# Kernel optimization log

Hardware: AMD Instinct MI355X
Metric: run time of the kernel (lower is better)

Reference implementation:

```python
import jax, jax.numpy as jnp
import numpy as np

D_MODEL, D_STATE, D_CONV, D_INNER = 1024, 16, 4, 2048
B, S = 1, 2048
EPS = 1e-5


def setup_inputs() -> dict:
    key = jax.random.key(0)
    ks = jax.random.split(key, 8)
    sc = 0.02
    return {
        "x": jax.random.normal(ks[0], (B, S, D_MODEL), jnp.float32),
        "ln_g": jnp.ones((D_MODEL,), jnp.float32),
        "ln_b": jnp.zeros((D_MODEL,), jnp.float32),
        "in_w": jax.random.normal(ks[1], (2 * D_INNER, D_MODEL), jnp.float32) * sc,
        "conv_w": jax.random.normal(ks[2], (D_INNER, 1, D_CONV), jnp.float32) * sc,  # depthwise OIH
        "conv_b": jax.random.normal(ks[3], (D_INNER,), jnp.float32) * sc,
        "xproj_w": jax.random.normal(ks[4], (2 * D_STATE + 1, D_INNER), jnp.float32) * sc,
        "dt_w": jax.random.normal(ks[5], (D_INNER, 1), jnp.float32) * sc,
        "dt_b": jax.random.normal(ks[6], (D_INNER,), jnp.float32) * sc,
        "A_log": jnp.log(jnp.arange(1, D_STATE + 1, dtype=jnp.float32)),
        "D": jnp.ones((D_INNER,), jnp.float32),
        "out_w": jax.random.normal(ks[7], (D_MODEL, D_INNER), jnp.float32) * sc,
    }


def reference(x, ln_g, ln_b, in_w, conv_w, conv_b, xproj_w, dt_w, dt_b, A_log, D, out_w):
    b, s, _ = x.shape
    d_inner = D.shape[0]
    d_state = A_log.shape[0]
    d_conv = conv_w.shape[-1]
    residual = x

    # LayerNorm
    mu = jnp.mean(x, axis=-1, keepdims=True)
    var = jnp.mean(jnp.square(x - mu), axis=-1, keepdims=True)
    xn = (x - mu) * jax.lax.rsqrt(var + EPS) * ln_g + ln_b

    # in_proj, split into x and gate z
    xz = jnp.einsum('bsd,ed->bse', xn, in_w)  # [B,S,2*d_inner]
    xi, z = jnp.split(xz, 2, axis=-1)

    # causal depthwise conv1d (torch pads d_conv-1 both sides then crops to seq_len)
    xc = jnp.transpose(xi, (0, 2, 1))  # [B,C,S]
    xc = jnp.pad(xc, ((0, 0), (0, 0), (d_conv - 1, 0)))
    xc = jax.lax.conv_general_dilated(
        xc, conv_w, window_strides=(1,), padding='VALID',
        dimension_numbers=('NCH', 'OIH', 'NCH'), feature_group_count=d_inner)
    xc = xc + conv_b[None, :, None]
    xs = jax.nn.silu(jnp.transpose(xc, (0, 2, 1)))  # [B,S,d_inner]

    # SSM projections
    xp = jnp.einsum('bsd,ed->bse', xs, xproj_w)  # [B,S,2*d_state+1]
    delta = jax.nn.softplus(xp[..., :1] * dt_w[:, 0] + dt_b)  # [B,S,d_inner]
    Bm = xp[..., 1:1 + d_state]  # [B,S,N]
    Cm = xp[..., 1 + d_state:]   # [B,S,N]
    A = -jnp.exp(A_log)          # [N]

    dA = jnp.exp(delta[..., None] * A)                      # [B,S,d_inner,N]
    dBx = delta[..., None] * Bm[:, :, None, :] * xs[..., None]  # [B,S,d_inner,N]

    def step(h, inp):
        dA_t, dBx_t, C_t = inp
        h = dA_t * h + dBx_t                     # [B,d_inner,N]
        y_t = jnp.einsum('bdn,bn->bd', h, C_t)   # [B,d_inner]
        return h, y_t

    h0 = jnp.zeros((b, d_inner, d_state), x.dtype)
    _, ys = jax.lax.scan(step, h0, (jnp.moveaxis(dA, 1, 0),
                                    jnp.moveaxis(dBx, 1, 0),
                                    jnp.moveaxis(Cm, 1, 0)))
    y = jnp.moveaxis(ys, 0, 1) + xs * D  # [B,S,d_inner]

    y = y * jax.nn.silu(z)
    out = jnp.einsum('bse,de->bsd', y, out_w)
    return out + residual
```

## Files before the change

kernel.cpp:

```cpp
#include <hip/hip_runtime.h>
#include <cstdint>
#include <cstddef>

#define D_MODEL 1024
#define D_STATE 16
#define D_CONV  4
#define D_INNER 2048
#define SEQ     2048
#define NCHUNK  128
#define CLEN    16
#define NGRP    8
#define GCH     16
#define LN_EPS  1e-5f

typedef unsigned short ushort_t;
typedef __attribute__((ext_vector_type(8))) short short8;
typedef __attribute__((ext_vector_type(4))) float f32x4;

__device__ __forceinline__ ushort_t f2bf(float x) {
  union { float f; uint32_t u; } v; v.f = x;
  uint32_t r = (v.u + 0x7fffu + ((v.u >> 16) & 1u)) >> 16;
  return (ushort_t)r;
}
__device__ __forceinline__ float bf2f(ushort_t u) {
  union { uint32_t x; float f; } v; v.x = ((uint32_t)u) << 16; return v.f;
}

__device__ __forceinline__ void async16(void* lds, const void* g) {
  __builtin_amdgcn_global_load_lds(
      (const __attribute__((address_space(1))) unsigned int*)g,
      (__attribute__((address_space(3))) unsigned int*)lds, 16, 0, 0);
}

__device__ __forceinline__ float softplus_f(float x) {
  if (x > 20.f) return x;
  if (x < -20.f) return __expf(x);
  return __logf(1.f + __expf(x));
}

__device__ __forceinline__ void dapow(float g1, float* da) {
  float g2 = g1 * g1, g4 = g2 * g2, g8 = g4 * g4;
  #pragma unroll
  for (int n = 0; n < 16; n++) {
    int e = n + 1;
    float v = (e & 1) ? g1 : 1.f;
    if (e & 2) v *= g2;
    if (e & 4) v *= g4;
    if (e & 8) v *= g8;
    da[n] = v;
  }
}

__global__ __launch_bounds__(256) void prep_kernel(const float* __restrict__ x,
                                                   const float* __restrict__ g,
                                                   const float* __restrict__ b,
                                                   const float* __restrict__ inw,
                                                   const float* __restrict__ outw,
                                                   const float* __restrict__ xpw,
                                                   ushort_t* __restrict__ xn_bf,
                                                   ushort_t* __restrict__ inw_bf,
                                                   ushort_t* __restrict__ outw_bf,
                                                   ushort_t* __restrict__ xpw_bf) {
  int blk = blockIdx.x;
  if (blk < SEQ) {
    int row = blk;
    const float4* xr = (const float4*)(x + (size_t)row * D_MODEL);
    float4 v = xr[threadIdx.x];
    float s  = v.x + v.y + v.z + v.w;
    float ss = v.x * v.x + v.y * v.y + v.z * v.z + v.w * v.w;
    #pragma unroll
    for (int o = 32; o; o >>= 1) { s += __shfl_down(s, o); ss += __shfl_down(ss, o); }
    __shared__ float sbuf[8], ssbuf[8];
    int wid = threadIdx.x >> 6, lane = threadIdx.x & 63;
    if (lane == 0) { sbuf[wid] = s; ssbuf[wid] = ss; }
    __syncthreads();
    if (threadIdx.x == 0) {
      float t = 0.f, t2 = 0.f;
      for (int i = 0; i < 4; i++) { t += sbuf[i]; t2 += ssbuf[i]; }
      float mu = t / D_MODEL;
      sbuf[4] = mu;
      ssbuf[4] = rsqrtf(t2 / D_MODEL - mu * mu + LN_EPS);
    }
    __syncthreads();
    float mu = sbuf[4], inv = ssbuf[4];
    float4 gv = ((const float4*)g)[threadIdx.x];
    float4 bv = ((const float4*)b)[threadIdx.x];
    ushort_t o4[4];
    o4[0] = f2bf((v.x - mu) * inv * gv.x + bv.x);
    o4[1] = f2bf((v.y - mu) * inv * gv.y + bv.y);
    o4[2] = f2bf((v.z - mu) * inv * gv.z + bv.z);
    o4[3] = f2bf((v.w - mu) * inv * gv.w + bv.w);
    *(ushort4*)&xn_bf[(size_t)row * D_MODEL + threadIdx.x * 4] =
        make_ushort4(o4[0], o4[1], o4[2], o4[3]);
  } else {
    int idx = ((blk - SEQ) * 256 + threadIdx.x) * 4;
    const int n1 = 2 * D_INNER * D_MODEL;
    const int n2 = D_MODEL * D_INNER;
    const int n3 = 64 * D_INNER;
    const float* src; ushort_t* dst; int j;
    if (idx < n1) { src = inw; dst = inw_bf; j = idx; }
    else if (idx < n1 + n2) { src = outw; dst = outw_bf; j = idx - n1; }
    else if (idx < n1 + n2 + n3) {
      j = idx - n1 - n2;
      if (j < 33 * D_INNER) { src = xpw; dst = xpw_bf; }
      else {
        *(ushort4*)&xpw_bf[j] = make_ushort4(0, 0, 0, 0);
        return;
      }
    } else return;
    float4 v = *(const float4*)&src[j];
    *(ushort4*)&dst[j] = make_ushort4(f2bf(v.x), f2bf(v.y), f2bf(v.z), f2bf(v.w));
  }
}

template <int BM, int BN, int KDIM, int EPI, int NBUF, int KSPLIT>
__global__ __launch_bounds__(256, 2) void gemm_pipe(const ushort_t* __restrict__ A,
                                                    const ushort_t* __restrict__ B,
                                                    void* __restrict__ Cout,
                                                    const float* __restrict__ R,
                                                    int N) {
  constexpr int KT = KDIM / 32 / KSPLIT;
  constexpr int K2 = KDIM * 2;
  constexpr int IA = BM / 64, IB = BN / 64;
  constexpr int S  = IA + IB;
  constexpr int W  = (NBUF - 2) * S;
  constexpr int WTM = BM / 2, WTN = BN / 2;
  constexpr int MREP = WTM / 16, NREP = WTN / 16;
  __shared__ __align__(16) ushort_t As[NBUF][BM * 32];
  __shared__ __align__(16) ushort_t Bs[NBUF][BN * 32];

  const int nwg = gridDim.x * gridDim.y;
  int bid = blockIdx.y * gridDim.x + blockIdx.x;
  int swz = (bid & 7) * (nwg >> 3) + (bid >> 3);
  int bn = swz % gridDim.x, bm = swz / gridDim.x;
  int ks = 0;
  if constexpr (KSPLIT > 1) { ks = bn; bn = 0; }
  const int tid = threadIdx.x, wid = tid >> 6, lane = tid & 63;
  const int wm = wid >> 1, wn = wid & 1;
  const int row0A = bm * BM, row0B = bn * BN;
  const size_t kbase = (size_t)ks * KT * 64;

  const char* gA[IA];
  const char* gB[IB];
  #pragma unroll
  for (int i = 0; i < IA; i++) {
    int o = i * 4096 + tid * 16;
    int r = o >> 6, src = (o & 63) ^ ((r & 3) << 4);
    gA[i] = (const char*)A + (size_t)(row0A + r) * K2 + src + kbase;
  }
  #pragma unroll
  for (int i = 0; i < IB; i++) {
    int o = i * 4096 + tid * 16;
    int r = o >> 6, src = (o & 63) ^ ((r & 3) << 4);
    gB[i] = (const char*)B + (size_t)(row0B + r) * K2 + src + kbase;
  }
  const int ldsW = wid * 1024;

  auto STAGE = [&](int bb, int kt) {
    int kb = kt * 64;
    #pragma unroll
    for (int i = 0; i < IA; i++)
      async16((char*)&As[bb][0] + i * 4096 + ldsW, gA[i] + kb);
    #pragma unroll
    for (int i = 0; i < IB; i++)
      async16((char*)&Bs[bb][0] + i * 4096 + ldsW, gB[i] + kb);
  };

  #pragma unroll
  for (int p = 0; p < NBUF - 1; p++) STAGE(p, p);

  int offA[MREP], offB[NREP];
  #pragma unroll
  for (int m = 0; m < MREP; m++) {
    int row = wm * WTM + m * 16 + (lane & 15);
    offA[m] = row * 64 + ((((lane >> 4)) ^ (row & 3)) << 4);
  }
  #pragma unroll
  for (int n = 0; n < NREP; n++) {
    int row = wn * WTN + n * 16 + (lane & 15);
    offB[n] = row * 64 + ((((lane >> 4)) ^ (row & 3)) << 4);
  }

  f32x4 acc[MREP][NREP] = {};
  int cur = 0;
  for (int kt = 0; kt < KT; kt++) {
    if (kt < KT - 1) {
      if constexpr (W == 6)       asm volatile("s_waitcnt vmcnt(6)" ::: "memory");
      else if constexpr (W == 8)  asm volatile("s_waitcnt vmcnt(8)" ::: "memory");
      else if constexpr (W == 12) asm volatile("s_waitcnt vmcnt(12)" ::: "memory");
      else                        asm volatile("s_waitcnt vmcnt(0)" ::: "memory");
    } else {
      asm volatile("s_waitcnt vmcnt(0)" ::: "memory");
    }
    __builtin_amdgcn_s_barrier();
    __builtin_amdgcn_sched_barrier(0);
    const char* Ab = (const char*)&As[cur][0];
    const char* Bb = (const char*)&Bs[cur][0];
    short8 af[MREP], bf[NREP];
    #pragma unroll
    for (int m = 0; m < MREP; m++) af[m] = *(const short8*)(Ab + offA[m]);
    #pragma unroll
    for (int n = 0; n < NREP; n++) bf[n] = *(const short8*)(Bb + offB[n]);
    if (kt + NBUF - 1 < KT) {
      int b2 = cur + NBUF - 1; if (b2 >= NBUF) b2 -= NBUF;
      STAGE(b2, kt + NBUF - 1);
    }
    __builtin_amdgcn_s_setprio(1);
    #pragma unroll
    for (int m = 0; m < MREP; m++)
      #pragma unroll
      for (int n = 0; n < NREP; n++)
        acc[m][n] = __builtin_amdgcn_mfma_f32_16x16x32_bf16(af[m], bf[n], acc[m][n], 0, 0, 0);
    __builtin_amdgcn_s_setprio(0);
    cur++; if (cur == NBUF) cur = 0;
  }

  #pragma unroll
  for (int m = 0; m < MREP; m++)
    #pragma unroll
    for (int n = 0; n < NREP; n++) {
      int r0 = row0A + wm * WTM + m * 16 + ((lane >> 4) << 2);
      int c  = row0B + wn * WTN + n * 16 + (lane & 15);
      #pragma unroll
      for (int q = 0; q < 4; q++) {
        if constexpr (EPI == 0) {
          ((ushort_t*)Cout)[(size_t)(r0 + q) * N + c] = f2bf(acc[m][n][q]);
        } else if constexpr (EPI == 1) {
          size_t idx = (size_t)(r0 + q) * N + c;
          ((float*)Cout)[idx] = acc[m][n][q] + R[idx];
        } else {
          if (c < 33)
            ((float*)Cout)[((size_t)ks * SEQ + r0 + q) * 33 + c] = acc[m][n][q];
        }
      }
    }
}

__global__ __launch_bounds__(256) void conv_silu_kernel(const ushort_t* __restrict__ xz_bf,
                                                        const float* __restrict__ cw,
                                                        const float* __restrict__ cb,
                                                        ushort_t* __restrict__ xs_bf) {
  const int t0 = blockIdx.x * 4;
  const int d0 = threadIdx.x * 8;
  short8 win[7];
  #pragma unroll
  for (int j = 0; j < 7; j++) {
    int tt = t0 - 3 + j;
    if (tt >= 0) win[j] = *(const short8*)&xz_bf[(size_t)tt * (2 * D_INNER) + d0];
    else         win[j] = (short8)0;
  }
  float4 w[8];
  float  cbv[8];
  #pragma unroll
  for (int j = 0; j < 8; j++) { w[j] = ((const float4*)cw)[d0 + j]; cbv[j] = cb[d0 + j]; }
  #pragma unroll
  for (int q = 0; q < 4; q++) {
    short8 o8;
    #pragma unroll
    for (int j = 0; j < 8; j++) {
      float acc = cbv[j]
                + bf2f((ushort_t)win[q][j])     * w[j].x
                + bf2f((ushort_t)win[q + 1][j]) * w[j].y
                + bf2f((ushort_t)win[q + 2][j]) * w[j].z
                + bf2f((ushort_t)win[q + 3][j]) * w[j].w;
      float sg = 1.f / (1.f + __expf(-acc));
      o8[j] = (short)f2bf(acc * sg);
    }
    *(short8*)&xs_bf[(size_t)(t0 + q) * D_INNER + d0] = o8;
  }
}

__global__ __launch_bounds__(256) void scan_pass1(const ushort_t* __restrict__ xs_bf,
                                                  const float* __restrict__ xpp,
                                                  const float* __restrict__ dt_w,
                                                  const float* __restrict__ dt_b,
                                                  const float* __restrict__ A_log,
                                                  ushort_t* __restrict__ Hp,
                                                  float* __restrict__ Sd) {
  int c = blockIdx.x;
  int d0 = blockIdx.y * 512 + threadIdx.x;
  __shared__ float Bsh[CLEN][16], drs[CLEN], Ash[16];
  {
    int t = threadIdx.x >> 4, n = threadIdx.x & 15;
    const size_t P = (size_t)SEQ * 33;
    size_t rb = (size_t)(c * CLEN + t) * 33;
    float sB = 0.f;
    #pragma unroll
    for (int k = 0; k < 8; k++) sB += xpp[k * P + rb + 1 + n];
    Bsh[t][n] = sB;
    if (threadIdx.x < CLEN) {
      size_t rr = (size_t)(c * CLEN + threadIdx.x) * 33;
      float sD = 0.f;
      #pragma unroll
      for (int k = 0; k < 8; k++) sD += xpp[k * P + rr];
      drs[threadIdx.x] = sD;
    } else if (threadIdx.x < CLEN + 16) {
      int n2 = threadIdx.x - CLEN;
      Ash[n2] = -__expf(A_log[n2]);
    }
  }
  __syncthreads();
  bool fastA = true;
  #pragma unroll
  for (int n = 0; n < 16; n++) fastA = fastA && (fabsf(Ash[n] + (float)(n + 1)) < 1e-4f * (n + 1));
  float dw[2] = {dt_w[d0], dt_w[d0 + 256]};
  float db[2] = {dt_b[d0], dt_b[d0 + 256]};
  float h[2][16] = {};
  float S[2] = {0.f, 0.f};
  size_t tb = (size_t)(c * CLEN) * D_INNER + d0;
  float xv[2] = {bf2f(xs_bf[tb]), bf2f(xs_bf[tb + 256])};
  for (int t = 0; t < CLEN; t++) {
    float nx[2] = {0.f, 0.f};
    if (t + 1 < CLEN) {
      nx[0] = bf2f(xs_bf[tb + D_INNER]);
      nx[1] = bf2f(xs_bf[tb + D_INNER + 256]);
    }
    float bb[16];
    *(float4*)&bb[0]  = *(const float4*)&Bsh[t][0];
    *(float4*)&bb[4]  = *(const float4*)&Bsh[t][4];
    *(float4*)&bb[8]  = *(const float4*)&Bsh[t][8];
    *(float4*)&bb[12] = *(const float4*)&Bsh[t][12];
    float drt = drs[t];
    #pragma unroll
    for (int u = 0; u < 2; u++) {
      float delta = softplus_f(drt * dw[u] + db[u]);
      S[u] += delta;
      float w = delta * xv[u];
      if (fastA) {
        float da[16];
        dapow(__expf(-delta), da);
        #pragma unroll
        for (int n = 0; n < 16; n++) h[u][n] = da[n] * h[u][n] + w * bb[n];
      } else {
        #pragma unroll
        for (int n = 0; n < 16; n++) h[u][n] = __expf(delta * Ash[n]) * h[u][n] + w * bb[n];
      }
    }
    xv[0] = nx[0]; xv[1] = nx[1];
    tb += D_INNER;
  }
  #pragma unroll
  for (int u = 0; u < 2; u++) {
    int d = d0 + u * 256;
    size_t base = ((size_t)c * D_INNER + d) * 16;
    short8 p0, p1;
    #pragma unroll
    for (int n = 0; n < 8; n++) { p0[n] = (short)f2bf(h[u][n]); p1[n] = (short)f2bf(h[u][8 + n]); }
    *(short8*)&Hp[base] = p0;
    *(short8*)&Hp[base + 8] = p1;
    Sd[(size_t)c * D_INNER + d] = S[u];
  }
}

__global__ __launch_bounds__(256) void combineA(const ushort_t* __restrict__ Hp,
                                                const float* __restrict__ Sd,
                                                const float* __restrict__ A_log,
                                                ushort_t* __restrict__ Hl,
                                                float* __restrict__ Slocp,
                                                ushort_t* __restrict__ Hgtot,
                                                float* __restrict__ Sgtot) {
  int g = blockIdx.x;
  int idx = blockIdx.y * 256 + threadIdx.x;
  int d = idx >> 4, n = idx & 15;
  float An = -__expf(A_log[n]);
  float h = 0.f, S = 0.f;
  const size_t stride = (size_t)D_INNER * 16;
  #pragma unroll 4
  for (int j = 0; j < GCH; j++) {
    int c = g * GCH + j;
    Hl[(size_t)c * stride + idx] = f2bf(h);
    if (n == 0) Slocp[(size_t)c * D_INNER + d] = S;
    float Sc = Sd[(size_t)c * D_INNER + d];
    float hp = bf2f(Hp[(size_t)c * stride + idx]);
    h = __expf(An * Sc) * h + hp;
    S += Sc;
  }
  Hgtot[(size_t)g * stride + idx] = f2bf(h);
  if (n == 0) Sgtot[(size_t)g * D_INNER + d] = S;
}

__global__ __launch_bounds__(256) void combineB(const ushort_t* __restrict__ Hgtot,
                                                const float* __restrict__ Sgtot,
                                                const float* __restrict__ A_log,
                                                ushort_t* __restrict__ Ginit) {
  int idx = blockIdx.x * 256 + threadIdx.x;
  int d = idx >> 4, n = idx & 15;
  float An = -__expf(A_log[n]);
  float G = 0.f;
  const size_t stride = (size_t)D_INNER * 16;
  #pragma unroll
  for (int g = 0; g < NGRP; g++) {
    Ginit[(size_t)g * stride + idx] = f2bf(G);
    G = __expf(An * Sgtot[(size_t)g * D_INNER + d]) * G + bf2f(Hgtot[(size_t)g * stride + idx]);
  }
}

__global__ __launch_bounds__(256) void scan_pass2(const ushort_t* __restrict__ xs_bf,
                                                  const float* __restrict__ xpp,
                                                  const ushort_t* __restrict__ xz_bf,
                                                  const float* __restrict__ dt_w,
                                                  const float* __restrict__ dt_b,
                                                  const float* __restrict__ A_log,
                                                  const float* __restrict__ Dp,
                                                  const ushort_t* __restrict__ Hl,
                                                  const float* __restrict__ Slocp,
                                                  const ushort_t* __restrict__ Ginit,
                                                  ushort_t* __restrict__ y_bf) {
  int c = blockIdx.x;
  int d0 = blockIdx.y * 512 + threadIdx.x;
  __shared__ float Bsh[CLEN][16], Csh[CLEN][16], drs[CLEN], Ash[16];
  {
    int t = threadIdx.x >> 4, n = threadIdx.x & 15;
    const size_t P = (size_t)SEQ * 33;
    size_t rb = (size_t)(c * CLEN + t) * 33;
    float sB = 0.f, sC = 0.f;
    #pragma unroll
    for (int k = 0; k < 8; k++) {
      sB += xpp[k * P + rb + 1 + n];
      sC += xpp[k * P + rb + 17 + n];
    }
    Bsh[t][n] = sB;
    Csh[t][n] = sC;
    if (threadIdx.x < CLEN) {
      size_t rr = (size_t)(c * CLEN + threadIdx.x) * 33;
      float sD = 0.f;
      #pragma unroll
      for (int k = 0; k < 8; k++) sD += xpp[k * P + rr];
      drs[threadIdx.x] = sD;
    } else if (threadIdx.x < CLEN + 16) {
      int n2 = threadIdx.x - CLEN;
      Ash[n2] = -__expf(A_log[n2]);
    }
  }
  __syncthreads();
  bool fastA = true;
  #pragma unroll
  for (int n = 0; n < 16; n++) fastA = fastA && (fabsf(Ash[n] + (float)(n + 1)) < 1e-4f * (n + 1));
  float dw[2] = {dt_w[d0], dt_w[d0 + 256]};
  float db[2] = {dt_b[d0], dt_b[d0 + 256]};
  float Dd[2] = {Dp[d0], Dp[d0 + 256]};
  int g8 = c >> 4;
  float h[2][16];
  #pragma unroll
  for (int u = 0; u < 2; u++) {
    int d = d0 + u * 256;
    size_t hb = ((size_t)c * D_INNER + d) * 16;
    size_t gb = ((size_t)g8 * D_INNER + d) * 16;
    float Slp = Slocp[(size_t)c * D_INNER + d];
    short8 hl0 = *(const short8*)&Hl[hb];
    short8 hl1 = *(const short8*)&Hl[hb + 8];
    short8 gi0 = *(const short8*)&Ginit[gb];
    short8 gi1 = *(const short8*)&Ginit[gb + 8];
    float hl[16], gi[16];
    #pragma unroll
    for (int n = 0; n < 8; n++) {
      hl[n] = bf2f((ushort_t)hl0[n]); hl[8 + n] = bf2f((ushort_t)hl1[n]);
      gi[n] = bf2f((ushort_t)gi0[n]); gi[8 + n] = bf2f((ushort_t)gi1[n]);
    }
    if (fastA) {
      float pw[16];
      dapow(__expf(-Slp), pw);
      #pragma unroll
      for (int n = 0; n < 16; n++) h[u][n] = hl[n] + pw[n] * gi[n];
    } else {
      #pragma unroll
      for (int n = 0; n < 16; n++) h[u][n] = hl[n] + __expf(Ash[n] * Slp) * gi[n];
    }
  }
  size_t tb = (size_t)(c * CLEN) * D_INNER + d0;
  size_t zb = (size_t)(c * CLEN) * (2 * D_INNER) + D_INNER + d0;
  float xv[2] = {bf2f(xs_bf[tb]), bf2f(xs_bf[tb + 256])};
  float zv[2] = {bf2f(xz_bf[zb]), bf2f(xz_bf[zb + 256])};
  for (int t = 0; t < CLEN; t++) {
    float nx[2] = {0.f, 0.f}, nz[2] = {0.f, 0.f};
    if (t + 1 < CLEN) {
      nx[0] = bf2f(xs_bf[tb + D_INNER]);
      nx[1] = bf2f(xs_bf[tb + D_INNER + 256]);
      nz[0] = bf2f(xz_bf[zb + 2 * D_INNER]);
      nz[1] = bf2f(xz_bf[zb + 2 * D_INNER + 256]);
    }
    float bb[16], cc[16];
    *(float4*)&bb[0]  = *(const float4*)&Bsh[t][0];
    *(float4*)&bb[4]  = *(const float4*)&Bsh[t][4];
    *(float4*)&bb[8]  = *(const float4*)&Bsh[t][8];
    *(float4*)&bb[12] = *(const float4*)&Bsh[t][12];
    *(float4*)&cc[0]  = *(const float4*)&Csh[t][0];
    *(float4*)&cc[4]  = *(const float4*)&Csh[t][4];
    *(float4*)&cc[8]  = *(const float4*)&Csh[t][8];
    *(float4*)&cc[12] = *(const float4*)&Csh[t][12];
    float drt = drs[t];
    size_t ti = (size_t)(c * CLEN + t);
    #pragma unroll
    for (int u = 0; u < 2; u++) {
      float delta = softplus_f(drt * dw[u] + db[u]);
      float w = delta * xv[u];
      float y = 0.f;
      if (fastA) {
        float da[16];
        dapow(__expf(-delta), da);
        #pragma unroll
        for (int n = 0; n < 16; n++) {
          h[u][n] = da[n] * h[u][n] + w * bb[n];
          y += h[u][n] * cc[n];
        }
      } else {
        #pragma unroll
        for (int n = 0; n < 16; n++) {
          h[u][n] = __expf(delta * Ash[n]) * h[u][n] + w * bb[n];
          y += h[u][n] * cc[n];
        }
      }
      float z = zv[u];
      float sz = z / (1.f + __expf(-z));
      float out = (y + xv[u] * Dd[u]) * sz;
      y_bf[ti * D_INNER + d0 + u * 256] = f2bf(out);
    }
    xv[0] = nx[0]; xv[1] = nx[1];
    zv[0] = nz[0]; zv[1] = nz[1];
    tb += D_INNER; zb += 2 * D_INNER;
  }
}

extern "C" void kernel_launch(void* const* d_in, const int* in_sizes, int n_in,
                              void* d_out, int out_size, void* d_ws, size_t ws_size,
                              hipStream_t stream) {
  const float* x      = (const float*)d_in[0];
  const float* ln_g   = (const float*)d_in[1];
  const float* ln_b   = (const float*)d_in[2];
  const float* in_w   = (const float*)d_in[3];
  const float* conv_w = (const float*)d_in[4];
  const float* conv_b = (const float*)d_in[5];
  const float* xproj_w= (const float*)d_in[6];
  const float* dt_w   = (const float*)d_in[7];
  const float* dt_b   = (const float*)d_in[8];
  const float* A_log  = (const float*)d_in[9];
  const float* Dp     = (const float*)d_in[10];
  const float* out_w  = (const float*)d_in[11];
  float* out = (float*)d_out;

  char* ws = (char*)d_ws;
  size_t off = 0;
  auto alloc = [&](size_t bytes) { char* p = ws + off; off += (bytes + 255) & ~(size_t)255; return p; };
  ushort_t* xz_bf   = (ushort_t*)alloc((size_t)SEQ * 2 * D_INNER * 2);
  ushort_t* xn_bf   = (ushort_t*)alloc((size_t)SEQ * D_MODEL * 2);
  ushort_t* inw_bf  = (ushort_t*)alloc((size_t)2 * D_INNER * D_MODEL * 2);
  ushort_t* outw_bf = (ushort_t*)alloc((size_t)D_MODEL * D_INNER * 2);
  ushort_t* xpw_bf  = (ushort_t*)alloc((size_t)64 * D_INNER * 2);
  ushort_t* xs_bf   = (ushort_t*)alloc((size_t)SEQ * D_INNER * 2);
  float*    xp_part = (float*)   alloc((size_t)8 * SEQ * 33 * 4);
  ushort_t* Hp      = (ushort_t*)alloc((size_t)NCHUNK * D_INNER * 16 * 2);
  ushort_t* Hl      = (ushort_t*)alloc((size_t)NCHUNK * D_INNER * 16 * 2);
  float*    Sd      = (float*)   alloc((size_t)NCHUNK * D_INNER * 4);
  float*    Slocp   = (float*)   alloc((size_t)NCHUNK * D_INNER * 4);
  ushort_t* Hgtot   = (ushort_t*)alloc((size_t)NGRP * D_INNER * 16 * 2);
  float*    Sgtot   = (float*)   alloc((size_t)NGRP * D_INNER * 4);
  ushort_t* Ginit   = (ushort_t*)alloc((size_t)NGRP * D_INNER * 16 * 2);
  ushort_t* y_bf    = (ushort_t*)alloc((size_t)SEQ * D_INNER * 2);
  (void)ws_size;

  const int ncvt4 = (2 * D_INNER * D_MODEL + D_MODEL * D_INNER + 64 * D_INNER) / 4;
  prep_kernel<<<SEQ + (ncvt4 + 255) / 256, 256, 0, stream>>>(
      x, ln_g, ln_b, in_w, out_w, xproj_w, xn_bf, inw_bf, outw_bf, xpw_bf);
  gemm_pipe<128, 128, D_MODEL, 0, 4, 1><<<dim3(2 * D_INNER / 128, SEQ / 128), 256, 0, stream>>>(
      xn_bf, inw_bf, xz_bf, nullptr, 2 * D_INNER);
  conv_silu_kernel<<<SEQ / 4, 256, 0, stream>>>(xz_bf, conv_w, conv_b, xs_bf);
  gemm_pipe<64, 64, D_INNER, 3, 6, 8><<<dim3(8, SEQ / 64), 256, 0, stream>>>(
      xs_bf, xpw_bf, xp_part, nullptr, 64);
  scan_pass1<<<dim3(NCHUNK, D_INNER / 512), 256, 0, stream>>>(xs_bf, xp_part, dt_w, dt_b, A_log, Hp, Sd);
  combineA<<<dim3(NGRP, D_INNER * 16 / 256), 256, 0, stream>>>(Hp, Sd, A_log, Hl, Slocp, Hgtot, Sgtot);
  combineB<<<D_INNER * 16 / 256, 256, 0, stream>>>(Hgtot, Sgtot, A_log, Ginit);
  scan_pass2<<<dim3(NCHUNK, D_INNER / 512), 256, 0, stream>>>(xs_bf, xp_part, xz_bf, dt_w, dt_b, A_log,
                                                              Dp, Hl, Slocp, Ginit, y_bf);
  gemm_pipe<64, 64, D_INNER, 1, 6, 1><<<dim3(D_MODEL / 64, SEQ / 64), 256, 0, stream>>>(
      y_bf, outw_bf, out, x, D_MODEL);
}
```

Before: 118.7 us.

## Fuse conv+SiLU into x_proj GEMM and fold combineB into scan_pass2

Measured after the change: 124.7 us. 1.05x slower.

```diff
diff --git a/kernel.cpp b/kernel.cpp
--- a/kernel.cpp
+++ b/kernel.cpp
@@ -225,49 +225,115 @@
       for (int q = 0; q < 4; q++) {
         if constexpr (EPI == 0) {
           ((ushort_t*)Cout)[(size_t)(r0 + q) * N + c] = f2bf(acc[m][n][q]);
-        } else if constexpr (EPI == 1) {
+        } else {
           size_t idx = (size_t)(r0 + q) * N + c;
           ((float*)Cout)[idx] = acc[m][n][q] + R[idx];
-        } else {
-          if (c < 33)
-            ((float*)Cout)[((size_t)ks * SEQ + r0 + q) * 33 + c] = acc[m][n][q];
         }
       }
     }
 }
 
-__global__ __launch_bounds__(256) void conv_silu_kernel(const ushort_t* __restrict__ xz_bf,
+__global__ __launch_bounds__(256) void convxproj_kernel(const ushort_t* __restrict__ xz_bf,
                                                         const float* __restrict__ cw,
                                                         const float* __restrict__ cb,
-                                                        ushort_t* __restrict__ xs_bf) {
-  const int t0 = blockIdx.x * 4;
-  const int d0 = threadIdx.x * 8;
-  short8 win[7];
-  #pragma unroll
-  for (int j = 0; j < 7; j++) {
-    int tt = t0 - 3 + j;
-    if (tt >= 0) win[j] = *(const short8*)&xz_bf[(size_t)tt * (2 * D_INNER) + d0];
-    else         win[j] = (short8)0;
-  }
-  float4 w[8];
-  float  cbv[8];
-  #pragma unroll
-  for (int j = 0; j < 8; j++) { w[j] = ((const float4*)cw)[d0 + j]; cbv[j] = cb[d0 + j]; }
-  #pragma unroll
-  for (int q = 0; q < 4; q++) {
+                                                        const ushort_t* __restrict__ xpw_bf,
+                                                        ushort_t* __restrict__ xs_bf,
+                                                        float* __restrict__ xp_part) {
+  constexpr int KT = 8;
+  __shared__ __align__(16) ushort_t As[2][64 * 32];
+  __shared__ __align__(16) ushort_t Bs[2][64 * 32];
+  const int ks = blockIdx.x, bm = blockIdx.y;
+  const int tid = threadIdx.x, wid = tid >> 6, lane = tid & 63;
+  const int wm = wid >> 1, wn = wid & 1;
+  const int row0A = bm * 64;
+  const int ar = tid >> 2, agc = tid & 3;
+  const int t = row0A + ar;
+  const int aws = ((agc ^ (ar & 3)) << 4);
+  const int bo = tid * 16;
+  const int br = bo >> 6;
+  const int bsrc = (bo & 63) ^ ((br & 3) << 4);
+  const char* gB = (const char*)xpw_bf + (size_t)br * (D_INNER * 2) + bsrc + (size_t)ks * KT * 64;
+
+  int offA[2], offB[2];
+  #pragma unroll
+  for (int m = 0; m < 2; m++) {
+    int row = wm * 32 + m * 16 + (lane & 15);
+    offA[m] = row * 64 + ((((lane >> 4)) ^ (row & 3)) << 4);
+  }
+  #pragma unroll
+  for (int n = 0; n < 2; n++) {
+    int row = wn * 32 + n * 16 + (lane & 15);
+    offB[n] = row * 64 + ((((lane >> 4)) ^ (row & 3)) << 4);
+  }
+
+  short8 xsv[KT];
+  auto STAGE = [&](int bb, int kt) {
+    async16((char*)&Bs[bb][0] + wid * 1024, gB + kt * 64);
+    int d0 = ks * 256 + kt * 32 + agc * 8;
+    short8 rv[4];
+    #pragma unroll
+    for (int j = 0; j < 4; j++) {
+      int tt = t - 3 + j;
+      if (tt >= 0) rv[j] = *(const short8*)&xz_bf[(size_t)tt * (2 * D_INNER) + d0];
+      else         rv[j] = (short8)0;
+    }
     short8 o8;
     #pragma unroll
-    for (int j = 0; j < 8; j++) {
-      float acc = cbv[j]
-                + bf2f((ushort_t)win[q][j])     * w[j].x
-                + bf2f((ushort_t)win[q + 1][j]) * w[j].y
-                + bf2f((ushort_t)win[q + 2][j]) * w[j].z
-                + bf2f((ushort_t)win[q + 3][j]) * w[j].w;
-      float sg = 1.f / (1.f + __expf(-acc));
-      o8[j] = (short)f2bf(acc * sg);
-    }
-    *(short8*)&xs_bf[(size_t)(t0 + q) * D_INNER + d0] = o8;
-  }
+    for (int jj = 0; jj < 8; jj++) {
+      float4 w4 = ((const float4*)cw)[d0 + jj];
+      float a = cb[d0 + jj]
+              + bf2f((ushort_t)rv[0][jj]) * w4.x
+              + bf2f((ushort_t)rv[1][jj]) * w4.y
+              + bf2f((ushort_t)rv[2][jj]) * w4.z
+              + bf2f((ushort_t)rv[3][jj]) * w4.w;
+      float sg = 1.f / (1.f + __expf(-a));
+      o8[jj] = (short)f2bf(a * sg);
+    }
+    *(short8*)((char*)&As[bb][0] + ar * 64 + aws) = o8;
+    return o8;
+  };
+
+  xsv[0] = STAGE(0, 0);
+  asm volatile("s_waitcnt vmcnt(0) lgkmcnt(0)" ::: "memory");
+  __builtin_amdgcn_s_barrier();
+
+  f32x4 acc[2][2] = {};
+  int cur = 0;
+  #pragma unroll
+  for (int kt = 0; kt < KT; kt++) {
+    short8 af[2], bfg[2];
+    #pragma unroll
+    for (int m = 0; m < 2; m++) af[m] = *(const short8*)((char*)&As[cur][0] + offA[m]);
+    #pragma unroll
+    for (int n = 0; n < 2; n++) bfg[n] = *(const short8*)((char*)&Bs[cur][0] + offB[n]);
+    if (kt + 1 < KT) xsv[kt + 1] = STAGE(cur ^ 1, kt + 1);
+    #pragma unroll
+    for (int m = 0; m < 2; m++)
+      #pragma unroll
+      for (int n = 0; n < 2; n++)
+        acc[m][n] = __builtin_amdgcn_mfma_f32_16x16x32_bf16(af[m], bfg[n], acc[m][n], 0, 0, 0);
+    asm volatile("s_waitcnt vmcnt(0) lgkmcnt(0)" ::: "memory");
+    __builtin_amdgcn_s_barrier();
+    cur ^= 1;
+  }
+
+  #pragma unroll
+  for (int kt = 0; kt < KT; kt++) {
+    int d0 = ks * 256 + kt * 32 + agc * 8;
+    *(short8*)&xs_bf[(size_t)t * D_INNER + d0] = xsv[kt];
+  }
+  #pragma unroll
+  for (int m = 0; m < 2; m++)
+    #pragma unroll
+    for (int n = 0; n < 2; n++) {
+      int r0 = row0A + wm * 32 + m * 16 + ((lane >> 4) << 2);
+      int c  = wn * 32 + n * 16 + (lane & 15);
+      if (c < 33) {
+        #pragma unroll
+        for (int q = 0; q < 4; q++)
+          xp_part[((size_t)ks * SEQ + r0 + q) * 33 + c] = acc[m][n][q];
+      }
+    }
 }
 
 __global__ __launch_bounds__(256) void scan_pass1(const ushort_t* __restrict__ xs_bf,
@@ -379,22 +445,6 @@
   if (n == 0) Sgtot[(size_t)g * D_INNER + d] = S;
 }
 
-__global__ __launch_bounds__(256) void combineB(const ushort_t* __restrict__ Hgtot,
-                                                const float* __restrict__ Sgtot,
-                                                const float* __restrict__ A_log,
-                                                ushort_t* __restrict__ Ginit) {
-  int idx = blockIdx.x * 256 + threadIdx.x;
-  int d = idx >> 4, n = idx & 15;
-  float An = -__expf(A_log[n]);
-  float G = 0.f;
-  const size_t stride = (size_t)D_INNER * 16;
-  #pragma unroll
-  for (int g = 0; g < NGRP; g++) {
-    Ginit[(size_t)g * stride + idx] = f2bf(G);
-    G = __expf(An * Sgtot[(size_t)g * D_INNER + d]) * G + bf2f(Hgtot[(size_t)g * stride + idx]);
-  }
-}
-
 __global__ __launch_bounds__(256) void scan_pass2(const ushort_t* __restrict__ xs_bf,
                                                   const float* __restrict__ xpp,
                                                   const ushort_t* __restrict__ xz_bf,
@@ -404,7 +454,8 @@
                                                   const float* __restrict__ Dp,
                                                   const ushort_t* __restrict__ Hl,
                                                   const float* __restrict__ Slocp,
-                                                  const ushort_t* __restrict__ Ginit,
+                                                  const ushort_t* __restrict__ Hgtot,
+                                                  const float* __restrict__ Sgtot,
                                                   ushort_t* __restrict__ y_bf) {
   int c = blockIdx.x;
   int d0 = blockIdx.y * 512 + threadIdx.x;
@@ -440,31 +491,52 @@
   float db[2] = {dt_b[d0], dt_b[d0 + 256]};
   float Dd[2] = {Dp[d0], Dp[d0 + 256]};
   int g8 = c >> 4;
+  const size_t stride = (size_t)D_INNER * 16;
   float h[2][16];
   #pragma unroll
   for (int u = 0; u < 2; u++) {
     int d = d0 + u * 256;
+    float G[16];
+    #pragma unroll
+    for (int n = 0; n < 16; n++) G[n] = 0.f;
+    for (int g = 0; g < g8; g++) {
+      float Sg = Sgtot[(size_t)g * D_INNER + d];
+      size_t gb = (size_t)g * stride + (size_t)d * 16;
+      short8 hg0 = *(const short8*)&Hgtot[gb];
+      short8 hg1 = *(const short8*)&Hgtot[gb + 8];
+      if (fastA) {
+        float pw[16];
+        dapow(__expf(-Sg), pw);
+        #pragma unroll
+        for (int n = 0; n < 8; n++) {
+          G[n]     = pw[n]     * G[n]     + bf2f((ushort_t)hg0[n]);
+          G[8 + n] = pw[8 + n] * G[8 + n] + bf2f((ushort_t)hg1[n]);
+        }
+      } else {
+        #pragma unroll
+        for (int n = 0; n < 8; n++) {
+          G[n]     = __expf(Ash[n] * Sg)     * G[n]     + bf2f((ushort_t)hg0[n]);
+          G[8 + n] = __expf(Ash[8 + n] * Sg) * G[8 + n] + bf2f((ushort_t)hg1[n]);
+        }
+      }
+    }
     size_t hb = ((size_t)c * D_INNER + d) * 16;
-    size_t gb = ((size_t)g8 * D_INNER + d) * 16;
     float Slp = Slocp[(size_t)c * D_INNER + d];
     short8 hl0 = *(const short8*)&Hl[hb];
     short8 hl1 = *(const short8*)&Hl[hb + 8];
-    short8 gi0 = *(const short8*)&Ginit[gb];
-    short8 gi1 = *(const short8*)&Ginit[gb + 8];
-    float hl[16], gi[16];
+    float hl[16];
     #pragma unroll
     for (int n = 0; n < 8; n++) {
       hl[n] = bf2f((ushort_t)hl0[n]); hl[8 + n] = bf2f((ushort_t)hl1[n]);
-      gi[n] = bf2f((ushort_t)gi0[n]); gi[8 + n] = bf2f((ushort_t)gi1[n]);
     }
     if (fastA) {
       float pw[16];
       dapow(__expf(-Slp), pw);
       #pragma unroll
-      for (int n = 0; n < 16; n++) h[u][n] = hl[n] + pw[n] * gi[n];
+      for (int n = 0; n < 16; n++) h[u][n] = hl[n] + pw[n] * G[n];
     } else {
       #pragma unroll
-      for (int n = 0; n < 16; n++) h[u][n] = hl[n] + __expf(Ash[n] * Slp) * gi[n];
+      for (int n = 0; n < 16; n++) h[u][n] = hl[n] + __expf(Ash[n] * Slp) * G[n];
     }
   }
   size_t tb = (size_t)(c * CLEN) * D_INNER + d0;
@@ -554,7 +626,6 @@
   float*    Slocp   = (float*)   alloc((size_t)NCHUNK * D_INNER * 4);
   ushort_t* Hgtot   = (ushort_t*)alloc((size_t)NGRP * D_INNER * 16 * 2);
   float*    Sgtot   = (float*)   alloc((size_t)NGRP * D_INNER * 4);
-  ushort_t* Ginit   = (ushort_t*)alloc((size_t)NGRP * D_INNER * 16 * 2);
   ushort_t* y_bf    = (ushort_t*)alloc((size_t)SEQ * D_INNER * 2);
   (void)ws_size;
 
@@ -563,14 +634,12 @@
       x, ln_g, ln_b, in_w, out_w, xproj_w, xn_bf, inw_bf, outw_bf, xpw_bf);
   gemm_pipe<128, 128, D_MODEL, 0, 4, 1><<<dim3(2 * D_INNER / 128, SEQ / 128), 256, 0, stream>>>(
       xn_bf, inw_bf, xz_bf, nullptr, 2 * D_INNER);
-  conv_silu_kernel<<<SEQ / 4, 256, 0, stream>>>(xz_bf, conv_w, conv_b, xs_bf);
-  gemm_pipe<64, 64, D_INNER, 3, 6, 8><<<dim3(8, SEQ / 64), 256, 0, stream>>>(
-      xs_bf, xpw_bf, xp_part, nullptr, 64);
+  convxproj_kernel<<<dim3(8, SEQ / 64), 256, 0, stream>>>(
+      xz_bf, conv_w, conv_b, xpw_bf, xs_bf, xp_part);
   scan_pass1<<<dim3(NCHUNK, D_INNER / 512), 256, 0, stream>>>(xs_bf, xp_part, dt_w, dt_b, A_log, Hp, Sd);
   combineA<<<dim3(NGRP, D_INNER * 16 / 256), 256, 0, stream>>>(Hp, Sd, A_log, Hl, Slocp, Hgtot, Sgtot);
-  combineB<<<D_INNER * 16 / 256, 256, 0, stream>>>(Hgtot, Sgtot, A_log, Ginit);
   scan_pass2<<<dim3(NCHUNK, D_INNER / 512), 256, 0, stream>>>(xs_bf, xp_part, xz_bf, dt_w, dt_b, A_log,
-                                                              Dp, Hl, Slocp, Ginit, y_bf);
+                                                              Dp, Hl, Slocp, Hgtot, Sgtot, y_bf);
   gemm_pipe<64, 64, D_INNER, 1, 6, 1><<<dim3(D_MODEL / 64, SEQ / 64), 256, 0, stream>>>(
       y_bf, outw_bf, out, x, D_MODEL);
 }
```

## Fold group-prefix combine into scan_pass2 and raise GEMM occupancy bounds

Applied to the files above, without the earlier changes.

Result: no change. 120.3 us (+1.4%).

```diff
diff --git a/kernel.cpp b/kernel.cpp
--- a/kernel.cpp
+++ b/kernel.cpp
@@ -113,12 +113,12 @@
   }
 }
 
-template <int BM, int BN, int KDIM, int EPI, int NBUF, int KSPLIT>
-__global__ __launch_bounds__(256, 2) void gemm_pipe(const ushort_t* __restrict__ A,
-                                                    const ushort_t* __restrict__ B,
-                                                    void* __restrict__ Cout,
-                                                    const float* __restrict__ R,
-                                                    int N) {
+template <int BM, int BN, int KDIM, int EPI, int NBUF, int KSPLIT, int MINW>
+__global__ __launch_bounds__(256, MINW) void gemm_pipe(const ushort_t* __restrict__ A,
+                                                       const ushort_t* __restrict__ B,
+                                                       void* __restrict__ Cout,
+                                                       const float* __restrict__ R,
+                                                       int N) {
   constexpr int KT = KDIM / 32 / KSPLIT;
   constexpr int K2 = KDIM * 2;
   constexpr int IA = BM / 64, IB = BN / 64;
@@ -185,7 +185,8 @@
   int cur = 0;
   for (int kt = 0; kt < KT; kt++) {
     if (kt < KT - 1) {
-      if constexpr (W == 6)       asm volatile("s_waitcnt vmcnt(6)" ::: "memory");
+      if constexpr (W == 4)       asm volatile("s_waitcnt vmcnt(4)" ::: "memory");
+      else if constexpr (W == 6)  asm volatile("s_waitcnt vmcnt(6)" ::: "memory");
       else if constexpr (W == 8)  asm volatile("s_waitcnt vmcnt(8)" ::: "memory");
       else if constexpr (W == 12) asm volatile("s_waitcnt vmcnt(12)" ::: "memory");
       else                        asm volatile("s_waitcnt vmcnt(0)" ::: "memory");
@@ -379,22 +380,6 @@
   if (n == 0) Sgtot[(size_t)g * D_INNER + d] = S;
 }
 
-__global__ __launch_bounds__(256) void combineB(const ushort_t* __restrict__ Hgtot,
-                                                const float* __restrict__ Sgtot,
-                                                const float* __restrict__ A_log,
-                                                ushort_t* __restrict__ Ginit) {
-  int idx = blockIdx.x * 256 + threadIdx.x;
-  int d = idx >> 4, n = idx & 15;
-  float An = -__expf(A_log[n]);
-  float G = 0.f;
-  const size_t stride = (size_t)D_INNER * 16;
-  #pragma unroll
-  for (int g = 0; g < NGRP; g++) {
-    Ginit[(size_t)g * stride + idx] = f2bf(G);
-    G = __expf(An * Sgtot[(size_t)g * D_INNER + d]) * G + bf2f(Hgtot[(size_t)g * stride + idx]);
-  }
-}
-
 __global__ __launch_bounds__(256) void scan_pass2(const ushort_t* __restrict__ xs_bf,
                                                   const float* __restrict__ xpp,
                                                   const ushort_t* __restrict__ xz_bf,
@@ -404,7 +389,8 @@
                                                   const float* __restrict__ Dp,
                                                   const ushort_t* __restrict__ Hl,
                                                   const float* __restrict__ Slocp,
-                                                  const ushort_t* __restrict__ Ginit,
+                                                  const ushort_t* __restrict__ Hgtot,
+                                                  const float* __restrict__ Sgtot,
                                                   ushort_t* __restrict__ y_bf) {
   int c = blockIdx.x;
   int d0 = blockIdx.y * 512 + threadIdx.x;
@@ -440,31 +426,52 @@
   float db[2] = {dt_b[d0], dt_b[d0 + 256]};
   float Dd[2] = {Dp[d0], Dp[d0 + 256]};
   int g8 = c >> 4;
+  const size_t stride = (size_t)D_INNER * 16;
   float h[2][16];
   #pragma unroll
   for (int u = 0; u < 2; u++) {
     int d = d0 + u * 256;
+    float G[16];
+    #pragma unroll
+    for (int n = 0; n < 16; n++) G[n] = 0.f;
+    for (int g = 0; g < g8; g++) {
+      float Sg = Sgtot[(size_t)g * D_INNER + d];
+      size_t gb = (size_t)g * stride + (size_t)d * 16;
+      short8 hg0 = *(const short8*)&Hgtot[gb];
+      short8 hg1 = *(const short8*)&Hgtot[gb + 8];
+      if (fastA) {
+        float pw[16];
+        dapow(__expf(-Sg), pw);
+        #pragma unroll
+        for (int n = 0; n < 8; n++) {
+          G[n]     = pw[n]     * G[n]     + bf2f((ushort_t)hg0[n]);
+          G[8 + n] = pw[8 + n] * G[8 + n] + bf2f((ushort_t)hg1[n]);
+        }
+      } else {
+        #pragma unroll
+        for (int n = 0; n < 8; n++) {
+          G[n]     = __expf(Ash[n] * Sg)     * G[n]     + bf2f((ushort_t)hg0[n]);
+          G[8 + n] = __expf(Ash[8 + n] * Sg) * G[8 + n] + bf2f((ushort_t)hg1[n]);
+        }
+      }
+    }
     size_t hb = ((size_t)c * D_INNER + d) * 16;
-    size_t gb = ((size_t)g8 * D_INNER + d) * 16;
     float Slp = Slocp[(size_t)c * D_INNER + d];
     short8 hl0 = *(const short8*)&Hl[hb];
     short8 hl1 = *(const short8*)&Hl[hb + 8];
-    short8 gi0 = *(const short8*)&Ginit[gb];
-    short8 gi1 = *(const short8*)&Ginit[gb + 8];
-    float hl[16], gi[16];
+    float hl[16];
     #pragma unroll
     for (int n = 0; n < 8; n++) {
       hl[n] = bf2f((ushort_t)hl0[n]); hl[8 + n] = bf2f((ushort_t)hl1[n]);
-      gi[n] = bf2f((ushort_t)gi0[n]); gi[8 + n] = bf2f((ushort_t)gi1[n]);
     }
     if (fastA) {
       float pw[16];
       dapow(__expf(-Slp), pw);
       #pragma unroll
-      for (int n = 0; n < 16; n++) h[u][n] = hl[n] + pw[n] * gi[n];
+      for (int n = 0; n < 16; n++) h[u][n] = hl[n] + pw[n] * G[n];
     } else {
       #pragma unroll
-      for (int n = 0; n < 16; n++) h[u][n] = hl[n] + __expf(Ash[n] * Slp) * gi[n];
+      for (int n = 0; n < 16; n++) h[u][n] = hl[n] + __expf(Ash[n] * Slp) * G[n];
     }
   }
   size_t tb = (size_t)(c * CLEN) * D_INNER + d0;
@@ -554,23 +561,21 @@
   float*    Slocp   = (float*)   alloc((size_t)NCHUNK * D_INNER * 4);
   ushort_t* Hgtot   = (ushort_t*)alloc((size_t)NGRP * D_INNER * 16 * 2);
   float*    Sgtot   = (float*)   alloc((size_t)NGRP * D_INNER * 4);
-  ushort_t* Ginit   = (ushort_t*)alloc((size_t)NGRP * D_INNER * 16 * 2);
   ushort_t* y_bf    = (ushort_t*)alloc((size_t)SEQ * D_INNER * 2);
   (void)ws_size;
 
   const int ncvt4 = (2 * D_INNER * D_MODEL + D_MODEL * D_INNER + 64 * D_INNER) / 4;
   prep_kernel<<<SEQ + (ncvt4 + 255) / 256, 256, 0, stream>>>(
       x, ln_g, ln_b, in_w, out_w, xproj_w, xn_bf, inw_bf, outw_bf, xpw_bf);
-  gemm_pipe<128, 128, D_MODEL, 0, 4, 1><<<dim3(2 * D_INNER / 128, SEQ / 128), 256, 0, stream>>>(
+  gemm_pipe<128, 128, D_MODEL, 0, 3, 1, 3><<<dim3(2 * D_INNER / 128, SEQ / 128), 256, 0, stream>>>(
       xn_bf, inw_bf, xz_bf, nullptr, 2 * D_INNER);
   conv_silu_kernel<<<SEQ / 4, 256, 0, stream>>>(xz_bf, conv_w, conv_b, xs_bf);
-  gemm_pipe<64, 64, D_INNER, 3, 6, 8><<<dim3(8, SEQ / 64), 256, 0, stream>>>(
+  gemm_pipe<64, 64, D_INNER, 3, 6, 8, 3><<<dim3(8, SEQ / 64), 256, 0, stream>>>(
       xs_bf, xpw_bf, xp_part, nullptr, 64);
   scan_pass1<<<dim3(NCHUNK, D_INNER / 512), 256, 0, stream>>>(xs_bf, xp_part, dt_w, dt_b, A_log, Hp, Sd);
   combineA<<<dim3(NGRP, D_INNER * 16 / 256), 256, 0, stream>>>(Hp, Sd, A_log, Hl, Slocp, Hgtot, Sgtot);
-  combineB<<<D_INNER * 16 / 256, 256, 0, stream>>>(Hgtot, Sgtot, A_log, Ginit);
   scan_pass2<<<dim3(NCHUNK, D_INNER / 512), 256, 0, stream>>>(xs_bf, xp_part, xz_bf, dt_w, dt_b, A_log,
-                                                              Dp, Hl, Slocp, Ginit, y_bf);
-  gemm_pipe<64, 64, D_INNER, 1, 6, 1><<<dim3(D_MODEL / 64, SEQ / 64), 256, 0, stream>>>(
+                                                              Dp, Hl, Slocp, Hgtot, Sgtot, y_bf);
+  gemm_pipe<64, 64, D_INNER, 1, 6, 1, 3><<<dim3(D_MODEL / 64, SEQ / 64), 256, 0, stream>>>(
       y_bf, outw_bf, out, x, D_MODEL);
 }
```
